# Kernel optimization log

Measured on AMD Instinct MI355X. Metric: run time of the kernel, lower is better.

The kernel has to match this reference:

```python
import jax, jax.numpy as jnp
import numpy as np
from jax import lax

FS, DW, CIN, COUT, NCLS, BATCH = 128, 8, 64, 256, 2, 512
K1, S1 = FS // 4, FS // 8          # 32, 16
L = FS * DW                        # 1024
T = (L - K1) // S1 + 1             # 63 SNN timesteps
BN_EPS = 1e-5


@jax.custom_vjp
def spike(u):
    """Heaviside spike on (v - threshold); surrogate grad exp(-|u|) (tau_grad=scale_grad=1)."""
    return (u >= 0).astype(u.dtype)

def _spike_fwd(u):
    return (u >= 0).astype(u.dtype), u

def _spike_bwd(u, g):
    return (g * jnp.exp(-jnp.abs(u)),)

spike.defvjp(_spike_fwd, _spike_bwd)


def cuba(x, threshold, current_decay, voltage_decay):
    """CUBA LIF scan. x: [N,C,T] -> binary spikes [N,C,T].
    i[t] = (1-cd)*i[t-1] + x[t]; v[t] = (1-vd)*v[t-1] + i[t]; s = v>=theta; v *= (1-s)."""
    cd, vd = 1.0 - current_decay, 1.0 - voltage_decay
    xs = jnp.moveaxis(x, -1, 0)  # [T,N,C]
    zero = jnp.zeros(x.shape[:-1], x.dtype)

    def step(carry, xt):
        i, v = carry
        i = cd * i + xt
        v = vd * v + i
        s = spike(v - threshold)
        v = v * (1.0 - s)
        return (i, v), s

    _, s = lax.scan(step, (zero, zero), xs)
    return jnp.moveaxis(s, 0, -1)


def conv1d(x, w, b, stride, pad):
    y = lax.conv_general_dilated(x, w, (stride,), [(pad, pad)],
                                 dimension_numbers=('NCH', 'OIH', 'NCH'))
    return y + b[None, :, None]


def bn(x, g, b, m, v):
    scale = g / jnp.sqrt(v + BN_EPS)
    return (x - m[None, :, None]) * scale[None, :, None] + b[None, :, None]


def setup_inputs() -> dict:
    key = jax.random.key(0)
    ks = jax.random.split(key, 12)
    return {
        'x':       jax.random.normal(ks[0], (BATCH, CIN, L), jnp.float32),
        'conv1_w': jax.random.normal(ks[1], (COUT, CIN, K1), jnp.float32) * 0.05,
        'conv1_b': jax.random.normal(ks[2], (COUT,), jnp.float32) * 0.05,
        'bn1_g':   jax.random.uniform(ks[3], (COUT,), jnp.float32, 0.5, 1.5),
        'bn1_b':   jax.random.normal(ks[4], (COUT,), jnp.float32) * 0.1,
        'bn1_m':   jax.random.normal(ks[5], (COUT,), jnp.float32) * 0.1,
        'bn1_v':   jax.random.uniform(ks[6], (COUT,), jnp.float32, 0.5, 1.5),
        'conv2_w': jax.random.normal(ks[7], (COUT, COUT, 3), jnp.float32) * 0.05,
        'conv2_b': jax.random.normal(ks[8], (COUT,), jnp.float32) * 0.05,
        'bn2_g':   jax.random.uniform(ks[9], (COUT,), jnp.float32, 0.5, 1.5),
        'bn2_b':   jax.random.normal(ks[10], (COUT,), jnp.float32) * 0.1,
        'bn2_m':   jax.random.normal(ks[11], (COUT,), jnp.float32) * 0.1,
        'bn2_v':   jax.random.uniform(jax.random.fold_in(key, 100), (COUT,), jnp.float32, 0.5, 1.5),
        'w1':      jax.random.normal(jax.random.fold_in(key, 101), (COUT, COUT), jnp.float32) * 0.1,
        'w2':      jax.random.normal(jax.random.fold_in(key, 102), (NCLS, COUT), jnp.float32) * 0.1,
    }


def reference(x, conv1_w, conv1_b, bn1_g, bn1_b, bn1_m, bn1_v,
              conv2_w, conv2_b, bn2_g, bn2_b, bn2_m, bn2_v, w1, w2):
    # CNN frontend (eval mode: BN uses running stats, dropout is identity)
    z = bn(conv1d(x, conv1_w, conv1_b, S1, 0), bn1_g, bn1_b, bn1_m, bn1_v)   # [N,COUT,T]
    z = bn(conv1d(z, conv2_w, conv2_b, 1, 1), bn2_g, bn2_b, bn2_m, bn2_v)    # [N,COUT,T]
    # CUBA Input encoder block: threshold=0.3, current_decay=0.9, voltage_decay=0.9
    z = cuba(z, 0.3, 0.9, 0.9)
    # CUBA Dense blocks (bias-free synapse per timestep + LIF): threshold=0.1, cd=1, vd=0.1
    z = cuba(jnp.einsum('oc,nct->not', w1, z), 0.1, 1.0, 0.1)
    z = cuba(jnp.einsum('oc,nct->not', w2, z), 0.1, 1.0, 0.1)
    return z  # binary spike trains [N, n_classes, T]
```

## Files before the change

kernel.cpp:

```cpp
#include <hip/hip_runtime.h>
#include <cstdint>
#include <cstddef>


typedef _Float16 half8 __attribute__((ext_vector_type(8)));
typedef float floatx4 __attribute__((ext_vector_type(4)));

__device__ __forceinline__ void split_f32(float v, _Float16& hi, _Float16& lo) {
    _Float16 h = (_Float16)v;
    hi = h;
    lo = (_Float16)((v - (float)h) * 2048.0f);
}

__global__ __launch_bounds__(256) void prep_kernel(
    const float* __restrict__ c1w, const float* __restrict__ c1b,
    const float* __restrict__ g1,  const float* __restrict__ b1,
    const float* __restrict__ m1,  const float* __restrict__ v1,
    const float* __restrict__ c2w, const float* __restrict__ c2b,
    const float* __restrict__ g2,  const float* __restrict__ b2,
    const float* __restrict__ m2,  const float* __restrict__ v2,
    const float* __restrict__ w1,
    float* __restrict__ w1T,
    _Float16* __restrict__ w1h, _Float16* __restrict__ w1l,
    _Float16* __restrict__ w2h, _Float16* __restrict__ w2l,
    float* __restrict__ ab1, float* __restrict__ ab2)
{
    const int id = blockIdx.x * 256 + threadIdx.x;
    if (id < 256) {
        float a1 = g1[id] / sqrtf(v1[id] + 1e-5f);
        ab1[id]       = a1;
        ab1[256 + id] = (c1b[id] - m1[id]) * a1 + b1[id];
        float a2 = g2[id] / sqrtf(v2[id] + 1e-5f);
        ab2[id]       = a2;
        ab2[256 + id] = (c2b[id] - m2[id]) * a2 + b2[id];
    }
    {
        const int c = id >> 8, o = id & 255;
        w1T[id] = w1[o * 256 + c];
    }
    for (int idx = id; idx < 256 * 2048; idx += 65536)
        split_f32(c1w[idx], w1h[idx], w1l[idx]);
    for (int idx = id; idx < 256 * 768; idx += 65536) {
        const int o  = idx / 768;
        const int r  = idx - o * 768;
        const int dt = r >> 8;
        const int c  = r & 255;
        split_f32(c2w[o * 768 + c * 3 + dt], w2h[idx], w2l[idx]);
    }
}

__global__ __launch_bounds__(256, 2) void conv1_mfma(
    const float* __restrict__ x,
    const _Float16* __restrict__ w1h, const _Float16* __restrict__ w1l,
    const float* __restrict__ ab,
    _Float16* __restrict__ z1h, _Float16* __restrict__ z1l)
{
    __shared__ _Float16 Ah[4][128][8];
    __shared__ _Float16 Al[4][128][8];
    __shared__ _Float16 Bh[4][128][8];
    __shared__ _Float16 Bl[4][128][8];

    const int tid = threadIdx.x;
    const int bm = blockIdx.x, bn = blockIdx.y;
    const int lr = tid & 127;
    const int h  = tid >> 7;

    const int am = bm * 128 + lr;
    const int an = am / 63, at = am - an * 63;
    const float*    arow  = x   + (size_t)an * 65536 + at * 16 + h * 16;
    const _Float16* bhrow = w1h + (size_t)(bn * 128 + lr) * 2048 + h * 16;
    const _Float16* blrow = w1l + (size_t)(bn * 128 + lr) * 2048 + h * 16;

    const int lane = tid & 63;
    const int wv   = tid >> 6;
    const int mw   = wv & 1, nw = wv >> 1;
    const int quad = lane >> 4;
    const int l15  = lane & 15;

    floatx4 accA[4][4] = {};
    floatx4 accB[4][4] = {};

    for (int it = 0; it < 64; ++it) {
        const float* ap = arow + it * 1024;
        float va[16];
        *(float4*)&va[0]  = *(const float4*)(ap);
        *(float4*)&va[4]  = *(const float4*)(ap + 4);
        *(float4*)&va[8]  = *(const float4*)(ap + 8);
        *(float4*)&va[12] = *(const float4*)(ap + 12);
        int4 bh0 = *(const int4*)(bhrow + it * 32);
        int4 bh1 = *(const int4*)(bhrow + it * 32 + 8);
        int4 bl0 = *(const int4*)(blrow + it * 32);
        int4 bl1 = *(const int4*)(blrow + it * 32 + 8);

        union U { _Float16 hf[8]; int4 v; };
        U c0h, c0l, c1h, c1l;
#pragma unroll
        for (int j = 0; j < 8; ++j) split_f32(va[j],     c0h.hf[j], c0l.hf[j]);
#pragma unroll
        for (int j = 0; j < 8; ++j) split_f32(va[8 + j], c1h.hf[j], c1l.hf[j]);

        __syncthreads();
        *(int4*)&Ah[2*h  ][lr][0] = c0h.v;
        *(int4*)&Ah[2*h+1][lr][0] = c1h.v;
        *(int4*)&Al[2*h  ][lr][0] = c0l.v;
        *(int4*)&Al[2*h+1][lr][0] = c1l.v;
        *(int4*)&Bh[2*h  ][lr][0] = bh0;
        *(int4*)&Bh[2*h+1][lr][0] = bh1;
        *(int4*)&Bl[2*h  ][lr][0] = bl0;
        *(int4*)&Bl[2*h+1][lr][0] = bl1;
        __syncthreads();

        half8 fah[4], fal[4], fbh[4], fbl[4];
#pragma unroll
        for (int t = 0; t < 4; ++t) {
            fah[t] = *(const half8*)&Ah[quad][mw*64 + t*16 + l15][0];
            fal[t] = *(const half8*)&Al[quad][mw*64 + t*16 + l15][0];
            fbh[t] = *(const half8*)&Bh[quad][nw*64 + t*16 + l15][0];
            fbl[t] = *(const half8*)&Bl[quad][nw*64 + t*16 + l15][0];
        }
#pragma unroll
        for (int ti = 0; ti < 4; ++ti)
#pragma unroll
            for (int tj = 0; tj < 4; ++tj) {
                accA[ti][tj] = __builtin_amdgcn_mfma_f32_16x16x32_f16(fah[ti], fbh[tj], accA[ti][tj], 0, 0, 0);
                accB[ti][tj] = __builtin_amdgcn_mfma_f32_16x16x32_f16(fah[ti], fbl[tj], accB[ti][tj], 0, 0, 0);
                accB[ti][tj] = __builtin_amdgcn_mfma_f32_16x16x32_f16(fal[ti], fbh[tj], accB[ti][tj], 0, 0, 0);
            }
    }

#pragma unroll
    for (int tj = 0; tj < 4; ++tj) {
        const int o = bn*128 + nw*64 + tj*16 + l15;
        const float alpha = ab[o], beta = ab[256 + o];
#pragma unroll
        for (int ti = 0; ti < 4; ++ti) {
            const int m0 = bm*128 + mw*64 + ti*16 + quad*4;
#pragma unroll
            for (int r = 0; r < 4; ++r) {
                float c = accA[ti][tj][r] + accB[ti][tj][r] * (1.0f/2048.0f);
                float z = c * alpha + beta;
                _Float16 zh, zl;
                split_f32(z, zh, zl);
                const size_t off = (size_t)(m0 + r) * 256 + o;
                z1h[off] = zh;
                z1l[off] = zl;
            }
        }
    }
}

__global__ __launch_bounds__(256, 2) void conv2_mfma(
    const _Float16* __restrict__ z1h, const _Float16* __restrict__ z1l,
    const _Float16* __restrict__ w2h, const _Float16* __restrict__ w2l,
    const float* __restrict__ ab, float* __restrict__ z2)
{
    __shared__ _Float16 Ah[4][128][8];
    __shared__ _Float16 Al[4][128][8];
    __shared__ _Float16 Bh[4][128][8];
    __shared__ _Float16 Bl[4][128][8];

    const int tid = threadIdx.x;
    const int bm = blockIdx.x, bn = blockIdx.y;
    const int lr = tid & 127;
    const int h  = tid >> 7;

    const int am = bm * 128 + lr;
    const int an = am / 63, at = am - an * 63;
    const _Float16* abase_h = z1h + (size_t)an * 16128;
    const _Float16* abase_l = z1l + (size_t)an * 16128;
    const _Float16* bhrow = w2h + (size_t)(bn * 128 + lr) * 768 + h * 16;
    const _Float16* blrow = w2l + (size_t)(bn * 128 + lr) * 768 + h * 16;

    const int lane = tid & 63;
    const int wv   = tid >> 6;
    const int mw   = wv & 1, nw = wv >> 1;
    const int quad = lane >> 4;
    const int l15  = lane & 15;

    floatx4 accA[4][4] = {};
    floatx4 accB[4][4] = {};

    const int4 z4 = {0, 0, 0, 0};

    for (int it = 0; it < 24; ++it) {
        const int kap0 = it * 32;
        const int dt   = kap0 >> 8;
        const int c0   = kap0 & 255;
        const int trow = at + dt - 1;
        const bool valid = (trow >= 0) && (trow < 63);
        const _Float16* aph = abase_h + trow * 256 + c0 + h * 16;
        const _Float16* apl = abase_l + trow * 256 + c0 + h * 16;
        int4 a0h = valid ? *(const int4*)(aph)     : z4;
        int4 a1h = valid ? *(const int4*)(aph + 8) : z4;
        int4 a0l = valid ? *(const int4*)(apl)     : z4;
        int4 a1l = valid ? *(const int4*)(apl + 8) : z4;
        int4 b0h = *(const int4*)(bhrow + kap0);
        int4 b1h = *(const int4*)(bhrow + kap0 + 8);
        int4 b0l = *(const int4*)(blrow + kap0);
        int4 b1l = *(const int4*)(blrow + kap0 + 8);

        __syncthreads();
        *(int4*)&Ah[2*h  ][lr][0] = a0h;
        *(int4*)&Ah[2*h+1][lr][0] = a1h;
        *(int4*)&Al[2*h  ][lr][0] = a0l;
        *(int4*)&Al[2*h+1][lr][0] = a1l;
        *(int4*)&Bh[2*h  ][lr][0] = b0h;
        *(int4*)&Bh[2*h+1][lr][0] = b1h;
        *(int4*)&Bl[2*h  ][lr][0] = b0l;
        *(int4*)&Bl[2*h+1][lr][0] = b1l;
        __syncthreads();

        half8 fah[4], fal[4], fbh[4], fbl[4];
#pragma unroll
        for (int t = 0; t < 4; ++t) {
            fah[t] = *(const half8*)&Ah[quad][mw*64 + t*16 + l15][0];
            fal[t] = *(const half8*)&Al[quad][mw*64 + t*16 + l15][0];
            fbh[t] = *(const half8*)&Bh[quad][nw*64 + t*16 + l15][0];
            fbl[t] = *(const half8*)&Bl[quad][nw*64 + t*16 + l15][0];
        }
#pragma unroll
        for (int ti = 0; ti < 4; ++ti)
#pragma unroll
            for (int tj = 0; tj < 4; ++tj) {
                accA[ti][tj] = __builtin_amdgcn_mfma_f32_16x16x32_f16(fah[ti], fbh[tj], accA[ti][tj], 0, 0, 0);
                accB[ti][tj] = __builtin_amdgcn_mfma_f32_16x16x32_f16(fah[ti], fbl[tj], accB[ti][tj], 0, 0, 0);
                accB[ti][tj] = __builtin_amdgcn_mfma_f32_16x16x32_f16(fal[ti], fbh[tj], accB[ti][tj], 0, 0, 0);
            }
    }

#pragma unroll
    for (int tj = 0; tj < 4; ++tj) {
        const int o = bn*128 + nw*64 + tj*16 + l15;
        const float alpha = ab[o], beta = ab[256 + o];
#pragma unroll
        for (int ti = 0; ti < 4; ++ti) {
            const int m0 = bm*128 + mw*64 + ti*16 + quad*4;
#pragma unroll
            for (int r = 0; r < 4; ++r) {
                float c = accA[ti][tj][r] + accB[ti][tj][r] * (1.0f/2048.0f);
                z2[(size_t)(m0 + r) * 256 + o] = c * alpha + beta;
            }
        }
    }
}

__global__ __launch_bounds__(256) void snn_fused(
    const float* __restrict__ z2, const float* __restrict__ w1T,
    const float* __restrict__ w2, float* __restrict__ out)
{
    __shared__ float Sc[256 * 16];
    __shared__ unsigned long long M2[256];
    __shared__ float Y[2 * 63];
    const int n   = blockIdx.x;
    const int tid = threadIdx.x;

    unsigned long long mask = 0ull;
    {
        float cur = 0.f, vol = 0.f;
        const float* zrow = z2 + (size_t)n * 16128 + tid;
        for (int t = 0; t < 63; ++t) {
            float xv = zrow[(size_t)t * 256];
            cur = 0.1f * cur + xv;
            vol = 0.1f * vol + cur;
            float u = vol - 0.3f;
            if (u >= 0.f) { mask |= (1ull << t); vol = 0.f; }
        }
    }

    unsigned long long mask2 = 0ull;
    float v2 = 0.f;
    for (int tc = 0; tc < 4; ++tc) {
        const int T0 = tc * 16;
        __syncthreads();
#pragma unroll
        for (int j4 = 0; j4 < 4; ++j4) {
            float4 f;
            f.x = ((mask >> (T0 + j4*4 + 0)) & 1ull) ? 1.f : 0.f;
            f.y = ((mask >> (T0 + j4*4 + 1)) & 1ull) ? 1.f : 0.f;
            f.z = ((mask >> (T0 + j4*4 + 2)) & 1ull) ? 1.f : 0.f;
            f.w = ((mask >> (T0 + j4*4 + 3)) & 1ull) ? 1.f : 0.f;
            *(float4*)&Sc[tid * 16 + j4 * 4] = f;
        }
        __syncthreads();
        float acc[16] = {};
        const float* wp = w1T + tid;
#pragma unroll 4
        for (int c = 0; c < 256; ++c) {
            float w = wp[(size_t)c * 256];
            const float* sp = &Sc[c * 16];
#pragma unroll
            for (int j = 0; j < 16; ++j) acc[j] += w * sp[j];
        }
        const int nT = (tc == 3) ? 15 : 16;
        for (int j = 0; j < nT; ++j) {
            v2 = 0.9f * v2 + acc[j];
            float u = v2 - 0.1f;
            if (u >= 0.f) { mask2 |= (1ull << (T0 + j)); v2 = 0.f; }
        }
    }
    __syncthreads();
    M2[tid] = mask2;
    __syncthreads();

    if (tid < 126) {
        const int cls = tid / 63;
        const int t   = tid - cls * 63;
        const float* wrow = w2 + cls * 256;
        float acc = 0.f;
#pragma unroll 4
        for (int o = 0; o < 256; ++o)
            acc += ((M2[o] >> t) & 1ull) ? wrow[o] : 0.f;
        Y[cls * 63 + t] = acc;
    }
    __syncthreads();
    if (tid < 2) {
        float v = 0.f;
        float* orow = out + (size_t)n * 126 + tid * 63;
        for (int t = 0; t < 63; ++t) {
            v = 0.9f * v + Y[tid * 63 + t];
            float u = v - 0.1f;
            float s = (u >= 0.f) ? 1.f : 0.f;
            orow[t] = s;
            v = (u >= 0.f) ? 0.f : v;
        }
    }
}

extern "C" void kernel_launch(void* const* d_in, const int* in_sizes, int n_in,
                              void* d_out, int out_size, void* d_ws, size_t ws_size,
                              hipStream_t stream)
{
    const float* x    = (const float*)d_in[0];
    const float* c1w  = (const float*)d_in[1];
    const float* c1b  = (const float*)d_in[2];
    const float* g1   = (const float*)d_in[3];
    const float* b1   = (const float*)d_in[4];
    const float* m1   = (const float*)d_in[5];
    const float* v1   = (const float*)d_in[6];
    const float* c2w  = (const float*)d_in[7];
    const float* c2b  = (const float*)d_in[8];
    const float* g2   = (const float*)d_in[9];
    const float* b2   = (const float*)d_in[10];
    const float* m2   = (const float*)d_in[11];
    const float* v2   = (const float*)d_in[12];
    const float* w1   = (const float*)d_in[13];
    const float* w2   = (const float*)d_in[14];
    float* out = (float*)d_out;

    float* ws = (float*)d_ws;
    float*    z2  = ws;
    _Float16* z1h = (_Float16*)(z2 + 8257536);
    _Float16* z1l = (_Float16*)(z2 + 8257536 + 4128768);
    float*    w1T = z2 + 8257536 + 2 * 4128768;
    _Float16* w1h = (_Float16*)(w1T + 65536);
    _Float16* w1l = (_Float16*)(w1T + 65536 + 262144);
    _Float16* w2h = (_Float16*)(w1T + 65536 + 2 * 262144);
    _Float16* w2l = (_Float16*)(w1T + 65536 + 2 * 262144 + 98304);
    float*    ab1 = w1T + 65536 + 2 * 262144 + 2 * 98304;
    float*    ab2 = ab1 + 512;

    prep_kernel<<<256, 256, 0, stream>>>(c1w, c1b, g1, b1, m1, v1,
                                         c2w, c2b, g2, b2, m2, v2,
                                         w1, w1T, w1h, w1l, w2h, w2l, ab1, ab2);
    conv1_mfma<<<dim3(252, 2), 256, 0, stream>>>(x, w1h, w1l, ab1, z1h, z1l);
    conv2_mfma<<<dim3(252, 2), 256, 0, stream>>>(z1h, z1l, w2h, w2l, ab2, z2);
    snn_fused<<<512, 256, 0, stream>>>(z2, w1T, w2, out);
}
```

Baseline: 483.6 us.

## Split SNN stage and run dense1 layer as split-fp16 MFMA GEMM

Replaces the fused SNN kernel, which did the 256x256 dense layer with scalar FP32 FMAs per sample, with three kernels. The first runs the first CUBA scan and writes fp16 spikes. The second does the dense layer as a batched MFMA GEMM, splitting the weights into hi/lo fp16 to keep close to fp32 accuracy. The tail runs the remaining LIF scans and the 2-class layer. This adds two launches and extra global round trips for spikes and y1, in exchange for moving the dense matmul onto matrix cores.

```diff
diff --git a/kernel.cpp b/kernel.cpp
--- a/kernel.cpp
+++ b/kernel.cpp
@@ -20,9 +20,9 @@
     const float* __restrict__ g2,  const float* __restrict__ b2,
     const float* __restrict__ m2,  const float* __restrict__ v2,
     const float* __restrict__ w1,
-    float* __restrict__ w1T,
     _Float16* __restrict__ w1h, _Float16* __restrict__ w1l,
     _Float16* __restrict__ w2h, _Float16* __restrict__ w2l,
+    _Float16* __restrict__ wdh, _Float16* __restrict__ wdl,
     float* __restrict__ ab1, float* __restrict__ ab2)
 {
     const int id = blockIdx.x * 256 + threadIdx.x;
@@ -34,10 +34,7 @@
         ab2[id]       = a2;
         ab2[256 + id] = (c2b[id] - m2[id]) * a2 + b2[id];
     }
-    {
-        const int c = id >> 8, o = id & 255;
-        w1T[id] = w1[o * 256 + c];
-    }
+    split_f32(w1[id], wdh[id], wdl[id]);
     for (int idx = id; idx < 256 * 2048; idx += 65536)
         split_f32(c1w[idx], w1h[idx], w1l[idx]);
     for (int idx = id; idx < 256 * 768; idx += 65536) {
@@ -244,62 +241,119 @@
     }
 }
 
-__global__ __launch_bounds__(256) void snn_fused(
-    const float* __restrict__ z2, const float* __restrict__ w1T,
-    const float* __restrict__ w2, float* __restrict__ out)
-{
-    __shared__ float Sc[256 * 16];
+__global__ __launch_bounds__(256) void cuba1_kernel(
+    const float* __restrict__ z2, _Float16* __restrict__ s1)
+{
+    const int n   = blockIdx.x;
+    const int tid = threadIdx.x;
+    const float* zrow = z2 + (size_t)n * 16128 + tid;
+    _Float16*    srow = s1 + (size_t)n * 16128 + tid;
+    float cur = 0.f, vol = 0.f;
+    for (int t = 0; t < 63; ++t) {
+        float xv = zrow[(size_t)t * 256];
+        cur = 0.1f * cur + xv;
+        vol = 0.1f * vol + cur;
+        bool sp = (vol - 0.3f) >= 0.f;
+        srow[(size_t)t * 256] = sp ? (_Float16)1.0f : (_Float16)0.0f;
+        if (sp) vol = 0.f;
+    }
+}
+
+__global__ __launch_bounds__(256, 2) void dense1_mfma(
+    const _Float16* __restrict__ s1,
+    const _Float16* __restrict__ wdh, const _Float16* __restrict__ wdl,
+    float* __restrict__ y1)
+{
+    __shared__ _Float16 As[4][128][8];
+    __shared__ _Float16 Bh[4][128][8];
+    __shared__ _Float16 Bl[4][128][8];
+
+    const int tid = threadIdx.x;
+    const int bm = blockIdx.x, bn = blockIdx.y;
+    const int lr = tid & 127;
+    const int h  = tid >> 7;
+
+    const _Float16* arow  = s1  + (size_t)(bm * 128 + lr) * 256 + h * 16;
+    const _Float16* bhrow = wdh + (size_t)(bn * 128 + lr) * 256 + h * 16;
+    const _Float16* blrow = wdl + (size_t)(bn * 128 + lr) * 256 + h * 16;
+
+    const int lane = tid & 63;
+    const int wv   = tid >> 6;
+    const int mw   = wv & 1, nw = wv >> 1;
+    const int quad = lane >> 4;
+    const int l15  = lane & 15;
+
+    floatx4 accA[4][4] = {};
+    floatx4 accB[4][4] = {};
+
+    for (int it = 0; it < 8; ++it) {
+        const int kap0 = it * 32;
+        int4 a0 = *(const int4*)(arow + kap0);
+        int4 a1 = *(const int4*)(arow + kap0 + 8);
+        int4 b0h = *(const int4*)(bhrow + kap0);
+        int4 b1h = *(const int4*)(bhrow + kap0 + 8);
+        int4 b0l = *(const int4*)(blrow + kap0);
+        int4 b1l = *(const int4*)(blrow + kap0 + 8);
+
+        __syncthreads();
+        *(int4*)&As[2*h  ][lr][0] = a0;
+        *(int4*)&As[2*h+1][lr][0] = a1;
+        *(int4*)&Bh[2*h  ][lr][0] = b0h;
+        *(int4*)&Bh[2*h+1][lr][0] = b1h;
+        *(int4*)&Bl[2*h  ][lr][0] = b0l;
+        *(int4*)&Bl[2*h+1][lr][0] = b1l;
+        __syncthreads();
+
+        half8 fa[4], fbh[4], fbl[4];
+#pragma unroll
+        for (int t = 0; t < 4; ++t) {
+            fa[t]  = *(const half8*)&As[quad][mw*64 + t*16 + l15][0];
+            fbh[t] = *(const half8*)&Bh[quad][nw*64 + t*16 + l15][0];
+            fbl[t] = *(const half8*)&Bl[quad][nw*64 + t*16 + l15][0];
+        }
+#pragma unroll
+        for (int ti = 0; ti < 4; ++ti)
+#pragma unroll
+            for (int tj = 0; tj < 4; ++tj) {
+                accA[ti][tj] = __builtin_amdgcn_mfma_f32_16x16x32_f16(fa[ti], fbh[tj], accA[ti][tj], 0, 0, 0);
+                accB[ti][tj] = __builtin_amdgcn_mfma_f32_16x16x32_f16(fa[ti], fbl[tj], accB[ti][tj], 0, 0, 0);
+            }
+    }
+
+#pragma unroll
+    for (int tj = 0; tj < 4; ++tj) {
+        const int o = bn*128 + nw*64 + tj*16 + l15;
+#pragma unroll
+        for (int ti = 0; ti < 4; ++ti) {
+            const int m0 = bm*128 + mw*64 + ti*16 + quad*4;
+#pragma unroll
+            for (int r = 0; r < 4; ++r)
+                y1[(size_t)(m0 + r) * 256 + o] =
+                    accA[ti][tj][r] + accB[ti][tj][r] * (1.0f/2048.0f);
+        }
+    }
+}
+
+__global__ __launch_bounds__(256) void snn_tail(
+    const float* __restrict__ y1, const float* __restrict__ w2,
+    float* __restrict__ out)
+{
     __shared__ unsigned long long M2[256];
     __shared__ float Y[2 * 63];
     const int n   = blockIdx.x;
     const int tid = threadIdx.x;
 
-    unsigned long long mask = 0ull;
     {
-        float cur = 0.f, vol = 0.f;
-        const float* zrow = z2 + (size_t)n * 16128 + tid;
+        const float* yrow = y1 + (size_t)n * 16128 + tid;
+        float v = 0.f;
+        unsigned long long mask2 = 0ull;
         for (int t = 0; t < 63; ++t) {
-            float xv = zrow[(size_t)t * 256];
-            cur = 0.1f * cur + xv;
-            vol = 0.1f * vol + cur;
-            float u = vol - 0.3f;
-            if (u >= 0.f) { mask |= (1ull << t); vol = 0.f; }
-        }
-    }
-
-    unsigned long long mask2 = 0ull;
-    float v2 = 0.f;
-    for (int tc = 0; tc < 4; ++tc) {
-        const int T0 = tc * 16;
-        __syncthreads();
-#pragma unroll
-        for (int j4 = 0; j4 < 4; ++j4) {
-            float4 f;
-            f.x = ((mask >> (T0 + j4*4 + 0)) & 1ull) ? 1.f : 0.f;
-            f.y = ((mask >> (T0 + j4*4 + 1)) & 1ull) ? 1.f : 0.f;
-            f.z = ((mask >> (T0 + j4*4 + 2)) & 1ull) ? 1.f : 0.f;
-            f.w = ((mask >> (T0 + j4*4 + 3)) & 1ull) ? 1.f : 0.f;
-            *(float4*)&Sc[tid * 16 + j4 * 4] = f;
-        }
-        __syncthreads();
-        float acc[16] = {};
-        const float* wp = w1T + tid;
-#pragma unroll 4
-        for (int c = 0; c < 256; ++c) {
-            float w = wp[(size_t)c * 256];
-            const float* sp = &Sc[c * 16];
-#pragma unroll
-            for (int j = 0; j < 16; ++j) acc[j] += w * sp[j];
-        }
-        const int nT = (tc == 3) ? 15 : 16;
-        for (int j = 0; j < nT; ++j) {
-            v2 = 0.9f * v2 + acc[j];
-            float u = v2 - 0.1f;
-            if (u >= 0.f) { mask2 |= (1ull << (T0 + j)); v2 = 0.f; }
-        }
-    }
-    __syncthreads();
-    M2[tid] = mask2;
+            float yv = yrow[(size_t)t * 256];
+            v = 0.9f * v + yv;
+            if ((v - 0.1f) >= 0.f) { mask2 |= (1ull << t); v = 0.f; }
+        }
+        M2[tid] = mask2;
+    }
     __syncthreads();
 
     if (tid < 126) {
@@ -348,21 +402,29 @@
     float* out = (float*)d_out;
 
     float* ws = (float*)d_ws;
-    float*    z2  = ws;
-    _Float16* z1h = (_Float16*)(z2 + 8257536);
-    _Float16* z1l = (_Float16*)(z2 + 8257536 + 4128768);
-    float*    w1T = z2 + 8257536 + 2 * 4128768;
-    _Float16* w1h = (_Float16*)(w1T + 65536);
-    _Float16* w1l = (_Float16*)(w1T + 65536 + 262144);
-    _Float16* w2h = (_Float16*)(w1T + 65536 + 2 * 262144);
-    _Float16* w2l = (_Float16*)(w1T + 65536 + 2 * 262144 + 98304);
-    float*    ab1 = w1T + 65536 + 2 * 262144 + 2 * 98304;
+    float*    zA  = ws;
+    _Float16* z1h = (_Float16*)zA;
+    _Float16* z1l = (_Float16*)(zA + 4128768);
+    float*    y1  = zA;
+    float*    z2  = zA + 8257536;
+    _Float16* s1  = (_Float16*)(z2 + 8257536);
+    float*    wsp = z2 + 8257536 + 4128768;
+    _Float16* w1h = (_Float16*)wsp;
+    _Float16* w1l = (_Float16*)(wsp + 262144);
+    _Float16* w2h = (_Float16*)(wsp + 2*262144);
+    _Float16* w2l = (_Float16*)(wsp + 2*262144 + 98304);
+    _Float16* wdh = (_Float16*)(wsp + 2*262144 + 2*98304);
+    _Float16* wdl = (_Float16*)(wsp + 2*262144 + 2*98304 + 32768);
+    float*    ab1 = wsp + 2*262144 + 2*98304 + 2*32768;
     float*    ab2 = ab1 + 512;
 
     prep_kernel<<<256, 256, 0, stream>>>(c1w, c1b, g1, b1, m1, v1,
                                          c2w, c2b, g2, b2, m2, v2,
-                                         w1, w1T, w1h, w1l, w2h, w2l, ab1, ab2);
+                                         w1, w1h, w1l, w2h, w2l, wdh, wdl,
+                                         ab1, ab2);
     conv1_mfma<<<dim3(252, 2), 256, 0, stream>>>(x, w1h, w1l, ab1, z1h, z1l);
     conv2_mfma<<<dim3(252, 2), 256, 0, stream>>>(z1h, z1l, w2h, w2l, ab2, z2);
-    snn_fused<<<512, 256, 0, stream>>>(z2, w1T, w2, out);
-}
+    cuba1_kernel<<<512, 256, 0, stream>>>(z2, s1);
+    dense1_mfma<<<dim3(252, 2), 256, 0, stream>>>(s1, wdh, wdl, y1);
+    snn_tail<<<512, 256, 0, stream>>>(y1, w2, out);
+}
```

Measured after the change: 433.3 us. 10.4% less time.
